# Optimization experiments

Measured on AMD Instinct MI355X. Metric: run time of the kernel, lower is better.

Reference implementation:

```python
import jax, jax.numpy as jnp
import numpy as np

N = 20000      # nodes in both graphs
B = 128        # graphs in batch
E = 320000     # edges (avg degree 16)
F_IN = 768     # num_features (bert/graph feature dim)
RAW_F = 5000   # raw feature dim (hardcoded 5000 in source)
H = 256        # nhid
C = 4          # num_classes


def _gcn(x, src, dst, W, b):
    # PyG GCNConv: add self loops, symmetric D^-1/2 (A+I) D^-1/2 normalization
    n = x.shape[0]
    h = x @ W
    loop = jnp.arange(n, dtype=src.dtype)
    s = jnp.concatenate([src, loop])
    d = jnp.concatenate([dst, loop])
    deg = jax.ops.segment_sum(jnp.ones_like(d, dtype=h.dtype), d, num_segments=n)
    dinv = jax.lax.rsqrt(jnp.maximum(deg, 1.0))
    norm = (dinv[s] * dinv[d])[:, None]
    out = jax.ops.segment_sum(h[s] * norm, d, num_segments=n)
    return out + b


def _segment_mean(x, seg, num_segments):
    s = jax.ops.segment_sum(x, seg, num_segments=num_segments)
    cnt = jax.ops.segment_sum(jnp.ones((x.shape[0],), x.dtype), seg, num_segments=num_segments)
    return s / jnp.maximum(cnt, 1.0)[:, None]


def _prelu(x, a):
    return jnp.where(x >= 0, x, a * x)


def setup_inputs():
    key = jax.random.key(0)
    k = jax.random.split(key, 16)
    graph_x = jax.random.normal(k[0], (N, F_IN), jnp.float32)
    bert_x = jax.random.normal(k[1], (N, F_IN), jnp.float32)
    data_x = jax.random.normal(k[2], (N, RAW_F), jnp.float32) * 0.05
    edge_index = jax.random.randint(k[3], (2, E), 0, N, jnp.int32)
    raw_edge_index = jax.random.randint(k[4], (2, E), 0, N, jnp.int32)
    batch = ((jnp.arange(N) * B) // N).astype(jnp.int32)  # sorted, covers all B graphs
    rootindex = jax.random.randint(k[5], (B,), 0, N, jnp.int32)

    def lin(kk, fin, fout):
        return jax.random.normal(kk, (fin, fout), jnp.float32) * (1.0 / np.sqrt(fin))

    W1 = lin(k[6], F_IN, H); b1 = jnp.zeros((H,), jnp.float32)
    Wc0 = lin(k[7], RAW_F, H); bc0 = jnp.zeros((H,), jnp.float32)
    Wc1 = lin(k[8], H, H); bc1 = jnp.zeros((H,), jnp.float32)
    Wc2 = lin(k[9], H, H); bc2 = jnp.zeros((H,), jnp.float32)
    Wl1 = lin(k[10], 2 * RAW_F, 2 * H); bl1 = jnp.zeros((2 * H,), jnp.float32)
    Wl2 = lin(k[11], 2 * H, H); bl2 = jnp.zeros((H,), jnp.float32)
    W5 = lin(k[12], 5 * H, C); b5 = jnp.zeros((C,), jnp.float32)
    prelu_a = jnp.asarray(0.25, jnp.float32)
    return dict(graph_x=graph_x, bert_x=bert_x, data_x=data_x,
                edge_index=edge_index, raw_edge_index=raw_edge_index,
                graph_batch=batch, x_batch=batch, rootindex=rootindex,
                W1=W1, b1=b1, Wc0=Wc0, bc0=bc0, Wc1=Wc1, bc1=bc1, Wc2=Wc2, bc2=bc2,
                Wl1=Wl1, bl1=bl1, Wl2=Wl2, bl2=bl2, prelu_a=prelu_a, W5=W5, b5=b5)


def reference(graph_x, bert_x, data_x, edge_index, raw_edge_index, graph_batch,
              x_batch, rootindex, W1, b1, Wc0, bc0, Wc1, bc1, Wc2, bc2,
              Wl1, bl1, Wl2, bl2, prelu_a, W5, b5):
    # branch 1: GCNConv over graph_x (bert_user=0), relu, global max pool
    x = jax.nn.relu(_gcn(graph_x, edge_index[0], edge_index[1], W1, b1))
    x = jax.ops.segment_max(x, graph_batch, num_segments=B)   # [B, H]
    # branch 2: scatter_mean of raw features + root node, MLP w/ PReLU (eval: dropout = id)
    new_x = _segment_mean(data_x, x_batch, B)                 # [B, RAW_F]
    root = data_x[rootindex]                                  # [B, RAW_F]
    new_x = jnp.concatenate([new_x, root], axis=1)            # [B, 2*RAW_F]
    new_x = _prelu(new_x @ Wl1 + bl1, prelu_a)
    new_x = _prelu(new_x @ Wl2 + bl2, prelu_a)                # [B, H]
    # branch 3 (boost=1): 3 GCN layers over raw graph, mean pool each layer
    x_one = data_x
    pools = []
    for (W, b) in ((Wc0, bc0), (Wc1, bc1), (Wc2, bc2)):
        x_one = jax.nn.relu(_gcn(x_one, raw_edge_index[0], raw_edge_index[1], W, b))
        pools.append(_segment_mean(x_one, x_batch, B))
    out = jnp.concatenate(pools + [new_x, x], axis=1)         # [B, 5*H]
    return jax.nn.log_softmax(out @ W5 + b5, axis=1)
```

## Files before the change

kernel.cpp:

```cpp
#include <hip/hip_runtime.h>
#include <math.h>

#define NN   20000
#define BG   128
#define EE   320000
#define FIN  768
#define RAWF 5000
#define KP   5120
#define CATK 10240
#define HD   256
#define NC   4

typedef __attribute__((ext_vector_type(4))) float          f32x4;
typedef __attribute__((ext_vector_type(8))) unsigned short u16x8;
typedef __attribute__((ext_vector_type(4))) unsigned short u16x4;
typedef __attribute__((ext_vector_type(8))) __bf16         bf16x8;

__device__ __forceinline__ unsigned short f2bf(float f) {
  unsigned u = __float_as_uint(f);
  u += 0x7FFFu + ((u >> 16) & 1u);
  return (unsigned short)(u >> 16);
}
__device__ __forceinline__ float bf2f(unsigned short u) {
  return __uint_as_float((unsigned)u << 16);
}

static inline int ceil_div(int a, int b) { return (a + b - 1) / b; }

__global__ void count_deg2_k(const int* __restrict__ ei, const int* __restrict__ rei,
                             int* __restrict__ deg1, int* __restrict__ deg2) {
  int i = blockIdx.x * 256 + threadIdx.x;
  if (i < EE) atomicAdd(&deg1[ei[EE + i]], 1);
  else if (i < 2 * EE) atomicAdd(&deg2[rei[i]], 1);
}

__global__ __launch_bounds__(1024) void scan_local_k(const int* __restrict__ deg1,
                                                     const int* __restrict__ deg2,
                                                     int* __restrict__ excl,
                                                     int* __restrict__ bsum, int nb) {
  const int* deg = blockIdx.y ? deg2 : deg1;
  int* ex = excl + (size_t)blockIdx.y * NN;
  int* bs = bsum + (size_t)blockIdx.y * nb;
  __shared__ int wsum[16];
  int t = threadIdx.x, lane = t & 63, w = t >> 6;
  int i = blockIdx.x * 1024 + t;
  int v = (i < NN) ? deg[i] : 0;
  int acc = v;
#pragma unroll
  for (int off = 1; off < 64; off <<= 1) {
    int o = __shfl_up(acc, off, 64);
    if (lane >= off) acc += o;
  }
  if (lane == 63) wsum[w] = acc;
  __syncthreads();
  if (w == 0 && lane < 16) {
    int s = wsum[lane];
#pragma unroll
    for (int off = 1; off < 16; off <<= 1) {
      int o = __shfl_up(s, off, 64);
      if (lane >= off) s += o;
    }
    wsum[lane] = s;
  }
  __syncthreads();
  if (w > 0) acc += wsum[w - 1];
  if (i < NN) ex[i] = acc - v;
  if (t == 1023) bs[blockIdx.x] = acc;
}

__global__ void scan_tops_k(const int* __restrict__ bsum, int* __restrict__ boff,
                            int* __restrict__ end1, int* __restrict__ end2, int nb) {
  int t = threadIdx.x;
  int half = t >> 5, idx = t & 31;
  int v = (idx < nb) ? bsum[half * nb + idx] : 0;
  int acc = v;
#pragma unroll
  for (int off = 1; off < 32; off <<= 1) {
    int o = __shfl_up(acc, off, 32);
    if (idx >= off) acc += o;
  }
  if (idx < nb) boff[half * nb + idx] = acc - v;
  if (idx == nb - 1) {
    if (half == 0) *end1 = acc; else *end2 = acc;
  }
}

__global__ __launch_bounds__(1024) void scan_add_k(
    const int* __restrict__ excl, const int* __restrict__ boff,
    const int* __restrict__ deg1, const int* __restrict__ deg2,
    int* __restrict__ rp1, int* __restrict__ rp2,
    int* __restrict__ cur1, int* __restrict__ cur2,
    float* __restrict__ dv1, float* __restrict__ dv2, int nb) {
  int y = blockIdx.y;
  const int* deg = y ? deg2 : deg1;
  int* rp = y ? rp2 : rp1;
  int* cur = y ? cur2 : cur1;
  float* dv = y ? dv2 : dv1;
  int i = blockIdx.x * 1024 + threadIdx.x;
  if (i < NN) {
    int v = excl[(size_t)y * NN + i] + boff[y * nb + blockIdx.x];
    rp[i] = v;
    cur[i] = v;
    dv[i] = rsqrtf((float)(deg[i] + 1));
  }
}

__global__ void scatter_k(const int* __restrict__ ei, const int* __restrict__ rei,
                          int* __restrict__ cur1, int* __restrict__ cur2,
                          int* __restrict__ col1, int* __restrict__ col2) {
  int i = blockIdx.x * 256 + threadIdx.x;
  int y = blockIdx.y;
  if (i < EE) {
    const int* e = y ? rei : ei;
    int* cur = y ? cur2 : cur1;
    int* col = y ? col2 : col1;
    int d = e[EE + i];
    int p = atomicAdd(&cur[d], 1);
    col[p] = e[i];
  }
}

__global__ void segbounds_k(const int* __restrict__ batch, int* __restrict__ s,
                            int* __restrict__ e, int n) {
  int i = blockIdx.x * 256 + threadIdx.x;
  if (i >= n) return;
  int b = batch[i];
  if (i == 0 || batch[i - 1] != b) s[b] = i;
  if (i == n - 1 || batch[i + 1] != b) e[b] = i + 1;
}

__global__ __launch_bounds__(256) void trans_k(
    const float* __restrict__ i0, unsigned short* __restrict__ o0,
    const float* __restrict__ i1, unsigned short* __restrict__ o1,
    const float* __restrict__ i2, unsigned short* __restrict__ o2,
    const float* __restrict__ i3, unsigned short* __restrict__ o3,
    const float* __restrict__ i4, unsigned short* __restrict__ o4) {
  __shared__ unsigned short tile[32][34];
  int b = blockIdx.x;
  const float* in; unsigned short* out;
  int K, N, Kout, tx, lid;
  if (b < 192)        { in=i0; out=o0; K=768;   N=256; Kout=768;   tx=24;  lid=b; }
  else if (b < 1472)  { in=i1; out=o1; K=5000;  N=256; Kout=5120;  tx=160; lid=b-192; }
  else if (b < 1536)  { in=i2; out=o2; K=256;   N=256; Kout=256;   tx=8;   lid=b-1472; }
  else if (b < 1600)  { in=i3; out=o3; K=256;   N=256; Kout=256;   tx=8;   lid=b-1536; }
  else                { in=i4; out=o4; K=10000; N=512; Kout=10240; tx=320; lid=b-1600; }
  int k0 = (lid % tx) * 32, n0 = (lid / tx) * 32;
  int txx = threadIdx.x & 31, tyy = threadIdx.x >> 5;
#pragma unroll
  for (int r = 0; r < 32; r += 8) {
    int k = k0 + tyy + r, n = n0 + txx;
    float v = (k < K) ? in[(size_t)k * N + n] : 0.f;
    tile[tyy + r][txx] = f2bf(v);
  }
  __syncthreads();
#pragma unroll
  for (int r = 0; r < 32; r += 8) {
    int n = n0 + tyy + r, k = k0 + txx;
    out[(size_t)n * Kout + k] = tile[txx][tyy + r];
  }
}

__global__ __launch_bounds__(256) void conv_pool_k(const float* __restrict__ x,
                                                   unsigned short* __restrict__ xb,
                                                   unsigned short* __restrict__ cat,
                                                   const int* __restrict__ segs,
                                                   const int* __restrict__ sege,
                                                   const int* __restrict__ root) {
  int g = blockIdx.x;
  if (blockIdx.y >= KP / 256) {
    int c = (blockIdx.y - KP / 256) * 256 + threadIdx.x;
    if (c < CATK - RAWF) {
      unsigned short v = 0;
      if (c < RAWF) v = f2bf(x[(size_t)root[g] * RAWF + c]);
      cat[(size_t)g * CATK + RAWF + c] = v;
    }
    return;
  }
  __shared__ f32x4 part[4][64];
  int wave = threadIdx.x >> 6, lane = threadIdx.x & 63;
  int c = blockIdx.y * 256 + lane * 4;
  int s = segs[g], e = sege[g];
  bool v4 = (c + 4 <= RAWF);
  f32x4 sum = (f32x4)0.f;
  for (int i = s + wave; i < e; i += 4) {
    f32x4 v = (f32x4)0.f;
    if (v4) v = *(const f32x4*)(x + (size_t)i * RAWF + c);
    if (xb) {
      u16x4 h;
      h[0] = f2bf(v[0]); h[1] = f2bf(v[1]); h[2] = f2bf(v[2]); h[3] = f2bf(v[3]);
      *(u16x4*)(xb + (size_t)i * KP + c) = h;
    }
    sum += v;
  }
  part[wave][lane] = sum;
  __syncthreads();
  if (threadIdx.x < 64 && v4) {
    f32x4 tot = part[0][lane] + part[1][lane] + part[2][lane] + part[3][lane];
    float cnt = (float)(e - s);
    u16x4 o;
    o[0] = f2bf(tot[0] / cnt); o[1] = f2bf(tot[1] / cnt);
    o[2] = f2bf(tot[2] / cnt); o[3] = f2bf(tot[3] / cnt);
    *(u16x4*)(cat + (size_t)g * CATK + c) = o;
  }
}

template <bool ABF16>
__global__ __launch_bounds__(256) void gemm_k(
    const void* __restrict__ Av, int Astride,
    const unsigned short* __restrict__ Bt, int Bstride,
    float* __restrict__ C, const float* __restrict__ escale,
    int M, int N, int Kreal, int kchunk, int atomic_out) {
  __shared__ unsigned short As[128 * 40];
  __shared__ unsigned short Bs[128 * 40];
  const int tid = threadIdx.x;
  const int lane = tid & 63, wave = tid >> 6;
  const int quad = lane >> 4, l16 = lane & 15;
  const int koff = quad * 8;

  int xt = blockIdx.x, yt = blockIdx.y;
  if (gridDim.x == 2) {
    const int MT = gridDim.y;
    int flat = (yt << 1) | xt;
    int gp = flat >> 4;
    int ybase = gp << 3;
    int rem = MT - ybase;
    int j = flat & 15;
    if (rem >= 8) { xt = j >> 3; yt = ybase + (j & 7); }
    else          { xt = (j >= rem); yt = ybase + (xt ? j - rem : j); }
  }
  const int bn = xt * 128, bm = yt * 128;
  const int wm = (wave >> 1) * 64, wn = (wave & 1) * 64;
  const int kbegin = blockIdx.z * kchunk;
  int kend = kbegin + kchunk; if (kend > Kreal) kend = Kreal;

  const int brow = tid >> 2, bcol = (tid & 3) * 8;
  const int arow_f = tid >> 3, acol_f = (tid & 7) * 4;

  u16x8 pb[2];
  u16x8 pa_b[2];
  f32x4 pa_f[4];

  auto load_tile = [&](int k0) {
#pragma unroll
    for (int i = 0; i < 2; ++i) {
      int gk = k0 + bcol;
      bool ok = ABF16 ? true : (gk + 8 <= kend);
      u16x8 v = (u16x8)(unsigned short)0;
      if (ok) v = *(const u16x8*)(Bt + (size_t)(bn + i * 64 + brow) * Bstride + gk);
      pb[i] = v;
    }
    if (ABF16) {
      const unsigned short* A = (const unsigned short*)Av;
#pragma unroll
      for (int i = 0; i < 2; ++i) {
        int r = bm + i * 64 + brow;
        u16x8 v = (u16x8)(unsigned short)0;
        if (r < M) v = *(const u16x8*)(A + (size_t)r * Astride + k0 + bcol);
        pa_b[i] = v;
      }
    } else {
      const float* A = (const float*)Av;
#pragma unroll
      for (int i = 0; i < 4; ++i) {
        int r = bm + i * 32 + arow_f;
        int gk = k0 + acol_f;
        f32x4 v = (f32x4)0.f;
        if (r < M && gk + 4 <= kend) v = *(const f32x4*)(A + (size_t)r * Astride + gk);
        pa_f[i] = v;
      }
    }
  };
  auto store_tile = [&]() {
#pragma unroll
    for (int i = 0; i < 2; ++i)
      *(u16x8*)&Bs[(i * 64 + brow) * 40 + bcol] = pb[i];
    if (ABF16) {
#pragma unroll
      for (int i = 0; i < 2; ++i)
        *(u16x8*)&As[(i * 64 + brow) * 40 + bcol] = pa_b[i];
    } else {
#pragma unroll
      for (int i = 0; i < 4; ++i) {
        u16x4 h;
        h[0] = f2bf(pa_f[i][0]); h[1] = f2bf(pa_f[i][1]);
        h[2] = f2bf(pa_f[i][2]); h[3] = f2bf(pa_f[i][3]);
        *(u16x4*)&As[(i * 32 + arow_f) * 40 + acol_f] = h;
      }
    }
  };

  f32x4 acc[4][4] = {};
  load_tile(kbegin);
  for (int k0 = kbegin; k0 < kend; k0 += 32) {
    store_tile();
    __syncthreads();
    int k1 = k0 + 32;
    if (k1 < kend) load_tile(k1);
    u16x8 ar[4], br[4];
#pragma unroll
    for (int i = 0; i < 4; ++i) ar[i] = *(const u16x8*)&As[(wm + i * 16 + l16) * 40 + koff];
#pragma unroll
    for (int j = 0; j < 4; ++j) br[j] = *(const u16x8*)&Bs[(wn + j * 16 + l16) * 40 + koff];
#pragma unroll
    for (int i = 0; i < 4; ++i)
#pragma unroll
      for (int j = 0; j < 4; ++j)
        acc[i][j] = __builtin_amdgcn_mfma_f32_16x16x32_bf16(
            __builtin_bit_cast(bf16x8, ar[i]), __builtin_bit_cast(bf16x8, br[j]),
            acc[i][j], 0, 0, 0);
    __syncthreads();
  }
#pragma unroll
  for (int i = 0; i < 4; ++i)
#pragma unroll
    for (int rr = 0; rr < 4; ++rr) {
      int grow = bm + wm + i * 16 + quad * 4 + rr;
      if (grow >= M) continue;
      float sc = escale ? escale[grow] : 1.f;
#pragma unroll
      for (int j = 0; j < 4; ++j) {
        int gcol = bn + wn + j * 16 + l16;
        if (gcol >= N) continue;
        float v = acc[i][j][rr] * sc;
        if (atomic_out) atomicAdd(&C[(size_t)grow * N + gcol], v);
        else C[(size_t)grow * N + gcol] = v;
      }
    }
}

__global__ __launch_bounds__(256) void gcn_agg_k(
    const float* __restrict__ h, const int* __restrict__ rowptr,
    const int* __restrict__ col, const float* __restrict__ dinv,
    const float* __restrict__ bias, unsigned short* __restrict__ outb, int n) {
  int wave = threadIdx.x >> 6, lane = threadIdx.x & 63;
  int node = blockIdx.x * 4 + wave;
  if (node >= n) return;
  int f = lane * 4;
  f32x4 acc = *(const f32x4*)(h + (size_t)node * HD + f);
  int beg = rowptr[node], end = rowptr[node + 1];
  int e = beg;
  for (; e + 4 <= end; e += 4) {
    int s0 = col[e], s1 = col[e + 1], s2 = col[e + 2], s3 = col[e + 3];
    f32x4 h0 = *(const f32x4*)(h + (size_t)s0 * HD + f);
    f32x4 h1 = *(const f32x4*)(h + (size_t)s1 * HD + f);
    f32x4 h2 = *(const f32x4*)(h + (size_t)s2 * HD + f);
    f32x4 h3 = *(const f32x4*)(h + (size_t)s3 * HD + f);
    acc += h0; acc += h1; acc += h2; acc += h3;
  }
  for (; e < end; ++e)
    acc += *(const f32x4*)(h + (size_t)col[e] * HD + f);
  float di = dinv[node];
  f32x4 b = *(const f32x4*)(bias + f);
  acc = acc * di + b;
  u16x4 o;
#pragma unroll
  for (int q = 0; q < 4; ++q) o[q] = f2bf(fmaxf(acc[q], 0.f));
  *(u16x4*)(outb + (size_t)node * HD + f) = o;
}

__global__ __launch_bounds__(256) void seg_pool_bf16_k(const unsigned short* __restrict__ src,
                                                       const int* __restrict__ segs,
                                                       const int* __restrict__ sege,
                                                       float* __restrict__ dst, int dstride,
                                                       int doff, int mode) {
  int g = blockIdx.x, f = threadIdx.x;
  int s = segs[g], e = sege[g];
  float a0, a1, a2, a3;
  if (mode == 1) { a0 = a1 = a2 = a3 = -INFINITY; } else { a0 = a1 = a2 = a3 = 0.f; }
  int i = s;
  for (; i + 4 <= e; i += 4) {
    float v0 = bf2f(src[(size_t)(i + 0) * HD + f]);
    float v1 = bf2f(src[(size_t)(i + 1) * HD + f]);
    float v2 = bf2f(src[(size_t)(i + 2) * HD + f]);
    float v3 = bf2f(src[(size_t)(i + 3) * HD + f]);
    if (mode == 1) { a0 = fmaxf(a0, v0); a1 = fmaxf(a1, v1); a2 = fmaxf(a2, v2); a3 = fmaxf(a3, v3); }
    else           { a0 += v0; a1 += v1; a2 += v2; a3 += v3; }
  }
  for (; i < e; ++i) {
    float v = bf2f(src[(size_t)i * HD + f]);
    if (mode == 1) a0 = fmaxf(a0, v); else a0 += v;
  }
  float acc;
  if (mode == 1) acc = fmaxf(fmaxf(a0, a1), fmaxf(a2, a3));
  else {
    acc = (a0 + a1) + (a2 + a3);
    acc /= (float)((e - s) > 0 ? (e - s) : 1);
  }
  dst[(size_t)g * dstride + doff + f] = acc;
}

__global__ __launch_bounds__(256) void gemm_e_k(const float* __restrict__ Cd,
                                                const float* __restrict__ bl1,
                                                const float* __restrict__ Wl2,
                                                const float* __restrict__ bl2,
                                                const float* __restrict__ pa,
                                                float* __restrict__ pools) {
  __shared__ float t[512];
  int b = blockIdx.x, n = threadIdx.x;
  float a = *pa;
  for (int k = n; k < 512; k += 256) {
    float v = Cd[(size_t)b * 512 + k] + bl1[k];
    t[k] = (v >= 0.f) ? v : a * v;
  }
  __syncthreads();
  float acc = 0.f;
  for (int k = 0; k < 512; ++k) acc = fmaf(t[k], Wl2[k * 256 + n], acc);
  acc += bl2[n];
  acc = (acc >= 0.f) ? acc : a * acc;
  pools[(size_t)b * 1280 + 768 + n] = acc;
}

__global__ __launch_bounds__(256) void final_k(const float* __restrict__ pools,
                                               const float* __restrict__ W5,
                                               const float* __restrict__ b5,
                                               float* __restrict__ out) {
  __shared__ float red[256][4];
  int b = blockIdx.x, t = threadIdx.x;
  float a0 = 0, a1 = 0, a2 = 0, a3 = 0;
  for (int i = t; i < 1280; i += 256) {
    float p = pools[(size_t)b * 1280 + i];
    a0 = fmaf(p, W5[i * 4 + 0], a0);
    a1 = fmaf(p, W5[i * 4 + 1], a1);
    a2 = fmaf(p, W5[i * 4 + 2], a2);
    a3 = fmaf(p, W5[i * 4 + 3], a3);
  }
  red[t][0] = a0; red[t][1] = a1; red[t][2] = a2; red[t][3] = a3;
  __syncthreads();
  for (int off = 128; off >= 1; off >>= 1) {
    if (t < off)
      for (int c = 0; c < 4; ++c) red[t][c] += red[t + off][c];
    __syncthreads();
  }
  if (t == 0) {
    float z[4];
    for (int c = 0; c < 4; ++c) z[c] = red[0][c] + b5[c];
    float m = fmaxf(fmaxf(z[0], z[1]), fmaxf(z[2], z[3]));
    float s = 0.f;
    for (int c = 0; c < 4; ++c) s += expf(z[c] - m);
    float lse = logf(s);
    for (int c = 0; c < 4; ++c) out[b * 4 + c] = z[c] - m - lse;
  }
}

extern "C" void kernel_launch(void* const* d_in, const int* in_sizes, int n_in,
                              void* d_out, int out_size, void* d_ws, size_t ws_size,
                              hipStream_t stream) {
  const float* graph_x = (const float*)d_in[0];
  const float* data_x  = (const float*)d_in[2];
  const int*   ei      = (const int*)d_in[3];
  const int*   rei     = (const int*)d_in[4];
  const int*   batch   = (const int*)d_in[5];
  const int*   rooti   = (const int*)d_in[7];
  const float* W1  = (const float*)d_in[8];   const float* b1  = (const float*)d_in[9];
  const float* Wc0 = (const float*)d_in[10];  const float* bc0 = (const float*)d_in[11];
  const float* Wc1 = (const float*)d_in[12];  const float* bc1 = (const float*)d_in[13];
  const float* Wc2 = (const float*)d_in[14];  const float* bc2 = (const float*)d_in[15];
  const float* Wl1 = (const float*)d_in[16];  const float* bl1 = (const float*)d_in[17];
  const float* Wl2 = (const float*)d_in[18];  const float* bl2 = (const float*)d_in[19];
  const float* pa  = (const float*)d_in[20];
  const float* W5  = (const float*)d_in[21];  const float* b5  = (const float*)d_in[22];
  float* out = (float*)d_out;

  char* ws = (char*)d_ws;
  size_t off = 0;
  auto take = [&](size_t bytes) -> void* {
    void* p = ws + off;
    off += (bytes + 255) & ~(size_t)255;
    return p;
  };
  const int NB = ceil_div(NN, 1024);

  int *deg1, *deg2, *rp1, *rp2, *cur1, *cur2, *col1, *col2, *excl, *bsum, *boff, *segs, *sege;
  float *dv1, *dv2, *hA, *Cd, *pools;
  unsigned short *W1t, *Wc0t, *Wc1t, *Wc2t, *Wl1t, *catb, *hBb, *Axb;

  auto alloc_all = [&](bool withAxb) {
    off = 0;
    deg1 = (int*)take(NN * 4);   deg2 = (int*)take(NN * 4);
    rp1  = (int*)take((NN + 1) * 4); rp2 = (int*)take((NN + 1) * 4);
    cur1 = (int*)take(NN * 4);   cur2 = (int*)take(NN * 4);
    col1 = (int*)take(EE * 4);   col2 = (int*)take(EE * 4);
    dv1  = (float*)take(NN * 4); dv2  = (float*)take(NN * 4);
    excl = (int*)take((size_t)2 * NN * 4);
    bsum = (int*)take(2 * NB * 4); boff = (int*)take(2 * NB * 4);
    segs = (int*)take(BG * 4);   sege = (int*)take(BG * 4);
    W1t  = (unsigned short*)take((size_t)HD * FIN * 2);
    Wc0t = (unsigned short*)take((size_t)HD * KP * 2);
    Wc1t = (unsigned short*)take((size_t)HD * HD * 2);
    Wc2t = (unsigned short*)take((size_t)HD * HD * 2);
    Wl1t = (unsigned short*)take((size_t)512 * CATK * 2);
    catb = (unsigned short*)take((size_t)BG * CATK * 2);
    Axb  = withAxb ? (unsigned short*)take((size_t)NN * KP * 2) : nullptr;
    hA   = (float*)take((size_t)NN * HD * 4);
    hBb  = (unsigned short*)take((size_t)NN * HD * 2);
    Cd   = (float*)take((size_t)BG * 512 * 4);
    pools = (float*)take((size_t)BG * 1280 * 4);
  };
  alloc_all(true);
  if (off > ws_size) alloc_all(false);
  const bool pathA = (Axb != nullptr);

  hipMemsetAsync(deg1, 0, (size_t)2 * ((NN * 4 + 255) & ~255), stream);
  hipMemsetAsync(Cd, 0, (size_t)BG * 512 * 4, stream);

  count_deg2_k<<<ceil_div(2 * EE, 256), 256, 0, stream>>>(ei, rei, deg1, deg2);
  scan_local_k<<<dim3(NB, 2), 1024, 0, stream>>>(deg1, deg2, excl, bsum, NB);
  scan_tops_k<<<1, 64, 0, stream>>>(bsum, boff, rp1 + NN, rp2 + NN, NB);
  scan_add_k<<<dim3(NB, 2), 1024, 0, stream>>>(excl, boff, deg1, deg2, rp1, rp2,
                                               cur1, cur2, dv1, dv2, NB);
  scatter_k<<<dim3(ceil_div(EE, 256), 2), 256, 0, stream>>>(ei, rei, cur1, cur2, col1, col2);
  segbounds_k<<<ceil_div(NN, 256), 256, 0, stream>>>(batch, segs, sege, NN);

  trans_k<<<6720, 256, 0, stream>>>(W1, W1t, Wc0, Wc0t, Wc1, Wc1t, Wc2, Wc2t, Wl1, Wl1t);

  conv_pool_k<<<dim3(BG, KP / 256 + ceil_div(CATK - RAWF, 256)), 256, 0, stream>>>(
      data_x, Axb, catb, segs, sege, rooti);

  int mt = ceil_div(NN, 128);

  hipMemsetAsync(hA, 0, (size_t)NN * HD * 4, stream);
  gemm_k<false><<<dim3(2, mt, 2), 256, 0, stream>>>(graph_x, FIN, W1t, FIN, hA, dv1,
                                                    NN, HD, FIN, 384, 1);
  gcn_agg_k<<<ceil_div(NN, 4), 256, 0, stream>>>(hA, rp1, col1, dv1, b1, hBb, NN);
  seg_pool_bf16_k<<<BG, 256, 0, stream>>>(hBb, segs, sege, pools, 1280, 1024, 1);

  hipMemsetAsync(hA, 0, (size_t)NN * HD * 4, stream);
  if (pathA)
    gemm_k<true><<<dim3(2, mt, 2), 256, 0, stream>>>(Axb, KP, Wc0t, KP, hA, dv2,
                                                     NN, HD, KP, 2560, 1);
  else
    gemm_k<false><<<dim3(2, mt, 4), 256, 0, stream>>>(data_x, RAWF, Wc0t, KP, hA, dv2,
                                                      NN, HD, RAWF, 1256, 1);
  gcn_agg_k<<<ceil_div(NN, 4), 256, 0, stream>>>(hA, rp2, col2, dv2, bc0, hBb, NN);
  seg_pool_bf16_k<<<BG, 256, 0, stream>>>(hBb, segs, sege, pools, 1280, 0, 0);

  hipMemsetAsync(hA, 0, (size_t)NN * HD * 4, stream);
  gemm_k<true><<<dim3(2, mt, 2), 256, 0, stream>>>(hBb, HD, Wc1t, HD, hA, dv2,
                                                   NN, HD, HD, 128, 1);
  gcn_agg_k<<<ceil_div(NN, 4), 256, 0, stream>>>(hA, rp2, col2, dv2, bc1, hBb, NN);
  seg_pool_bf16_k<<<BG, 256, 0, stream>>>(hBb, segs, sege, pools, 1280, 256, 0);

  hipMemsetAsync(hA, 0, (size_t)NN * HD * 4, stream);
  gemm_k<true><<<dim3(2, mt, 2), 256, 0, stream>>>(hBb, HD, Wc2t, HD, hA, dv2,
                                                   NN, HD, HD, 128, 1);
  gcn_agg_k<<<ceil_div(NN, 4), 256, 0, stream>>>(hA, rp2, col2, dv2, bc2, hBb, NN);
  seg_pool_bf16_k<<<BG, 256, 0, stream>>>(hBb, segs, sege, pools, 1280, 512, 0);

  gemm_k<true><<<dim3(4, 1, 32), 256, 0, stream>>>(catb, CATK, Wl1t, CATK, Cd, nullptr,
                                                   BG, 512, CATK, 320, 1);
  gemm_e_k<<<BG, 256, 0, stream>>>(Cd, bl1, Wl2, bl2, pa, pools);

  final_k<<<BG, 256, 0, stream>>>(pools, W5, b5, out);
}
```

Baseline: 1.356 ms.

## Store GCN hidden features as bf16 and drop split-K atomics on small GEMMs

The small GEMMs (W1, Wc1, Wc2) now run without split-K and write scaled outputs directly as bf16, removing three memsets and the fp32 atomic adds. The Wc0 GEMM keeps split-K into fp32 and is followed by a new conversion kernel to bf16. The aggregation kernel then gathers bf16 rows, halving gather traffic. The segbounds kernel is folded into scan_add, the two memsets are merged by making Cd contiguous with the degree arrays, and one split-K chunk size is changed. Fewer GEMM blocks may lower parallelism, and bf16 intermediates reduce precision.

After: 1.198 ms. 11.7% less time.

```diff
diff --git a/kernel.cpp b/kernel.cpp
--- a/kernel.cpp
+++ b/kernel.cpp
@@ -90,7 +90,9 @@
     const int* __restrict__ deg1, const int* __restrict__ deg2,
     int* __restrict__ rp1, int* __restrict__ rp2,
     int* __restrict__ cur1, int* __restrict__ cur2,
-    float* __restrict__ dv1, float* __restrict__ dv2, int nb) {
+    float* __restrict__ dv1, float* __restrict__ dv2,
+    const int* __restrict__ batch, int* __restrict__ segs, int* __restrict__ sege,
+    int nb) {
   int y = blockIdx.y;
   const int* deg = y ? deg2 : deg1;
   int* rp = y ? rp2 : rp1;
@@ -102,6 +104,11 @@
     rp[i] = v;
     cur[i] = v;
     dv[i] = rsqrtf((float)(deg[i] + 1));
+    if (y == 0) {
+      int b = batch[i];
+      if (i == 0 || batch[i - 1] != b) segs[b] = i;
+      if (i == NN - 1 || batch[i + 1] != b) sege[b] = i + 1;
+    }
   }
 }
 
@@ -118,15 +125,6 @@
     int p = atomicAdd(&cur[d], 1);
     col[p] = e[i];
   }
-}
-
-__global__ void segbounds_k(const int* __restrict__ batch, int* __restrict__ s,
-                            int* __restrict__ e, int n) {
-  int i = blockIdx.x * 256 + threadIdx.x;
-  if (i >= n) return;
-  int b = batch[i];
-  if (i == 0 || batch[i - 1] != b) s[b] = i;
-  if (i == n - 1 || batch[i + 1] != b) e[b] = i + 1;
 }
 
 __global__ __launch_bounds__(256) void trans_k(
@@ -208,7 +206,8 @@
 __global__ __launch_bounds__(256) void gemm_k(
     const void* __restrict__ Av, int Astride,
     const unsigned short* __restrict__ Bt, int Bstride,
-    float* __restrict__ C, const float* __restrict__ escale,
+    float* __restrict__ C, unsigned short* __restrict__ Cb,
+    const float* __restrict__ escale,
     int M, int N, int Kreal, int kchunk, int atomic_out) {
   __shared__ unsigned short As[128 * 40];
   __shared__ unsigned short Bs[128 * 40];
@@ -322,33 +321,51 @@
         int gcol = bn + wn + j * 16 + l16;
         if (gcol >= N) continue;
         float v = acc[i][j][rr] * sc;
-        if (atomic_out) atomicAdd(&C[(size_t)grow * N + gcol], v);
+        if (Cb) Cb[(size_t)grow * N + gcol] = f2bf(v);
+        else if (atomic_out) atomicAdd(&C[(size_t)grow * N + gcol], v);
         else C[(size_t)grow * N + gcol] = v;
       }
     }
 }
 
+__global__ void conv_h_k(const float* __restrict__ in, unsigned short* __restrict__ out) {
+  size_t i = (size_t)(blockIdx.x * 256 + threadIdx.x) * 8;
+  f32x4 a = *(const f32x4*)(in + i);
+  f32x4 b = *(const f32x4*)(in + i + 4);
+  u16x8 o;
+  o[0]=f2bf(a[0]); o[1]=f2bf(a[1]); o[2]=f2bf(a[2]); o[3]=f2bf(a[3]);
+  o[4]=f2bf(b[0]); o[5]=f2bf(b[1]); o[6]=f2bf(b[2]); o[7]=f2bf(b[3]);
+  *(u16x8*)(out + i) = o;
+}
+
 __global__ __launch_bounds__(256) void gcn_agg_k(
-    const float* __restrict__ h, const int* __restrict__ rowptr,
+    const unsigned short* __restrict__ hb, const int* __restrict__ rowptr,
     const int* __restrict__ col, const float* __restrict__ dinv,
     const float* __restrict__ bias, unsigned short* __restrict__ outb, int n) {
   int wave = threadIdx.x >> 6, lane = threadIdx.x & 63;
   int node = blockIdx.x * 4 + wave;
   if (node >= n) return;
   int f = lane * 4;
-  f32x4 acc = *(const f32x4*)(h + (size_t)node * HD + f);
+  u16x4 sv = *(const u16x4*)(hb + (size_t)node * HD + f);
+  f32x4 acc;
+  acc[0] = bf2f(sv[0]); acc[1] = bf2f(sv[1]); acc[2] = bf2f(sv[2]); acc[3] = bf2f(sv[3]);
   int beg = rowptr[node], end = rowptr[node + 1];
   int e = beg;
   for (; e + 4 <= end; e += 4) {
     int s0 = col[e], s1 = col[e + 1], s2 = col[e + 2], s3 = col[e + 3];
-    f32x4 h0 = *(const f32x4*)(h + (size_t)s0 * HD + f);
-    f32x4 h1 = *(const f32x4*)(h + (size_t)s1 * HD + f);
-    f32x4 h2 = *(const f32x4*)(h + (size_t)s2 * HD + f);
-    f32x4 h3 = *(const f32x4*)(h + (size_t)s3 * HD + f);
-    acc += h0; acc += h1; acc += h2; acc += h3;
-  }
-  for (; e < end; ++e)
-    acc += *(const f32x4*)(h + (size_t)col[e] * HD + f);
+    u16x4 h0 = *(const u16x4*)(hb + (size_t)s0 * HD + f);
+    u16x4 h1 = *(const u16x4*)(hb + (size_t)s1 * HD + f);
+    u16x4 h2 = *(const u16x4*)(hb + (size_t)s2 * HD + f);
+    u16x4 h3 = *(const u16x4*)(hb + (size_t)s3 * HD + f);
+#pragma unroll
+    for (int q = 0; q < 4; ++q)
+      acc[q] += bf2f(h0[q]) + bf2f(h1[q]) + bf2f(h2[q]) + bf2f(h3[q]);
+  }
+  for (; e < end; ++e) {
+    u16x4 h0 = *(const u16x4*)(hb + (size_t)col[e] * HD + f);
+#pragma unroll
+    for (int q = 0; q < 4; ++q) acc[q] += bf2f(h0[q]);
+  }
   float di = dinv[node];
   f32x4 b = *(const f32x4*)(bias + f);
   acc = acc * di + b;
@@ -472,11 +489,12 @@
 
   int *deg1, *deg2, *rp1, *rp2, *cur1, *cur2, *col1, *col2, *excl, *bsum, *boff, *segs, *sege;
   float *dv1, *dv2, *hA, *Cd, *pools;
-  unsigned short *W1t, *Wc0t, *Wc1t, *Wc2t, *Wl1t, *catb, *hBb, *Axb;
+  unsigned short *W1t, *Wc0t, *Wc1t, *Wc2t, *Wl1t, *catb, *hAb, *hBb, *Axb;
 
   auto alloc_all = [&](bool withAxb) {
     off = 0;
     deg1 = (int*)take(NN * 4);   deg2 = (int*)take(NN * 4);
+    Cd   = (float*)take((size_t)BG * 512 * 4);
     rp1  = (int*)take((NN + 1) * 4); rp2 = (int*)take((NN + 1) * 4);
     cur1 = (int*)take(NN * 4);   cur2 = (int*)take(NN * 4);
     col1 = (int*)take(EE * 4);   col2 = (int*)take(EE * 4);
@@ -492,24 +510,24 @@
     catb = (unsigned short*)take((size_t)BG * CATK * 2);
     Axb  = withAxb ? (unsigned short*)take((size_t)NN * KP * 2) : nullptr;
     hA   = (float*)take((size_t)NN * HD * 4);
+    hAb  = (unsigned short*)take((size_t)NN * HD * 2);
     hBb  = (unsigned short*)take((size_t)NN * HD * 2);
-    Cd   = (float*)take((size_t)BG * 512 * 4);
     pools = (float*)take((size_t)BG * 1280 * 4);
   };
   alloc_all(true);
   if (off > ws_size) alloc_all(false);
   const bool pathA = (Axb != nullptr);
 
-  hipMemsetAsync(deg1, 0, (size_t)2 * ((NN * 4 + 255) & ~255), stream);
-  hipMemsetAsync(Cd, 0, (size_t)BG * 512 * 4, stream);
+  const size_t degpad = ((size_t)NN * 4 + 255) & ~(size_t)255;
+  hipMemsetAsync(deg1, 0, degpad * 2 + (size_t)BG * 512 * 4, stream);
 
   count_deg2_k<<<ceil_div(2 * EE, 256), 256, 0, stream>>>(ei, rei, deg1, deg2);
   scan_local_k<<<dim3(NB, 2), 1024, 0, stream>>>(deg1, deg2, excl, bsum, NB);
   scan_tops_k<<<1, 64, 0, stream>>>(bsum, boff, rp1 + NN, rp2 + NN, NB);
   scan_add_k<<<dim3(NB, 2), 1024, 0, stream>>>(excl, boff, deg1, deg2, rp1, rp2,
-                                               cur1, cur2, dv1, dv2, NB);
+                                               cur1, cur2, dv1, dv2,
+                                               batch, segs, sege, NB);
   scatter_k<<<dim3(ceil_div(EE, 256), 2), 256, 0, stream>>>(ei, rei, cur1, cur2, col1, col2);
-  segbounds_k<<<ceil_div(NN, 256), 256, 0, stream>>>(batch, segs, sege, NN);
 
   trans_k<<<6720, 256, 0, stream>>>(W1, W1t, Wc0, Wc0t, Wc1, Wc1t, Wc2, Wc2t, Wl1, Wl1t);
 
@@ -518,35 +536,36 @@
 
   int mt = ceil_div(NN, 128);
 
-  hipMemsetAsync(hA, 0, (size_t)NN * HD * 4, stream);
-  gemm_k<false><<<dim3(2, mt, 2), 256, 0, stream>>>(graph_x, FIN, W1t, FIN, hA, dv1,
-                                                    NN, HD, FIN, 384, 1);
-  gcn_agg_k<<<ceil_div(NN, 4), 256, 0, stream>>>(hA, rp1, col1, dv1, b1, hBb, NN);
+  gemm_k<false><<<dim3(2, mt, 1), 256, 0, stream>>>(graph_x, FIN, W1t, FIN,
+                                                    nullptr, hAb, dv1,
+                                                    NN, HD, FIN, FIN, 0);
+  gcn_agg_k<<<ceil_div(NN, 4), 256, 0, stream>>>(hAb, rp1, col1, dv1, b1, hBb, NN);
   seg_pool_bf16_k<<<BG, 256, 0, stream>>>(hBb, segs, sege, pools, 1280, 1024, 1);
 
   hipMemsetAsync(hA, 0, (size_t)NN * HD * 4, stream);
   if (pathA)
-    gemm_k<true><<<dim3(2, mt, 2), 256, 0, stream>>>(Axb, KP, Wc0t, KP, hA, dv2,
+    gemm_k<true><<<dim3(2, mt, 2), 256, 0, stream>>>(Axb, KP, Wc0t, KP, hA, nullptr, dv2,
                                                      NN, HD, KP, 2560, 1);
   else
-    gemm_k<false><<<dim3(2, mt, 4), 256, 0, stream>>>(data_x, RAWF, Wc0t, KP, hA, dv2,
-                                                      NN, HD, RAWF, 1256, 1);
-  gcn_agg_k<<<ceil_div(NN, 4), 256, 0, stream>>>(hA, rp2, col2, dv2, bc0, hBb, NN);
+    gemm_k<false><<<dim3(2, mt, 4), 256, 0, stream>>>(data_x, RAWF, Wc0t, KP, hA, nullptr, dv2,
+                                                      NN, HD, RAWF, 1280, 1);
+  conv_h_k<<<(NN * HD) / (256 * 8), 256, 0, stream>>>(hA, hAb);
+  gcn_agg_k<<<ceil_div(NN, 4), 256, 0, stream>>>(hAb, rp2, col2, dv2, bc0, hBb, NN);
   seg_pool_bf16_k<<<BG, 256, 0, stream>>>(hBb, segs, sege, pools, 1280, 0, 0);
 
-  hipMemsetAsync(hA, 0, (size_t)NN * HD * 4, stream);
-  gemm_k<true><<<dim3(2, mt, 2), 256, 0, stream>>>(hBb, HD, Wc1t, HD, hA, dv2,
-                                                   NN, HD, HD, 128, 1);
-  gcn_agg_k<<<ceil_div(NN, 4), 256, 0, stream>>>(hA, rp2, col2, dv2, bc1, hBb, NN);
+  gemm_k<true><<<dim3(2, mt, 1), 256, 0, stream>>>(hBb, HD, Wc1t, HD,
+                                                   nullptr, hAb, dv2,
+                                                   NN, HD, HD, HD, 0);
+  gcn_agg_k<<<ceil_div(NN, 4), 256, 0, stream>>>(hAb, rp2, col2, dv2, bc1, hBb, NN);
   seg_pool_bf16_k<<<BG, 256, 0, stream>>>(hBb, segs, sege, pools, 1280, 256, 0);
 
-  hipMemsetAsync(hA, 0, (size_t)NN * HD * 4, stream);
-  gemm_k<true><<<dim3(2, mt, 2), 256, 0, stream>>>(hBb, HD, Wc2t, HD, hA, dv2,
-                                                   NN, HD, HD, 128, 1);
-  gcn_agg_k<<<ceil_div(NN, 4), 256, 0, stream>>>(hA, rp2, col2, dv2, bc2, hBb, NN);
+  gemm_k<true><<<dim3(2, mt, 1), 256, 0, stream>>>(hBb, HD, Wc2t, HD,
+                                                   nullptr, hAb, dv2,
+                                                   NN, HD, HD, HD, 0);
+  gcn_agg_k<<<ceil_div(NN, 4), 256, 0, stream>>>(hAb, rp2, col2, dv2, bc2, hBb, NN);
   seg_pool_bf16_k<<<BG, 256, 0, stream>>>(hBb, segs, sege, pools, 1280, 512, 0);
 
-  gemm_k<true><<<dim3(4, 1, 32), 256, 0, stream>>>(catb, CATK, Wl1t, CATK, Cd, nullptr,
+  gemm_k<true><<<dim3(4, 1, 32), 256, 0, stream>>>(catb, CATK, Wl1t, CATK, Cd, nullptr, nullptr,
                                                    BG, 512, CATK, 320, 1);
   gemm_e_k<<<BG, 256, 0, stream>>>(Cd, bl1, Wl2, bl2, pa, pools);
 
```
